# Performance work log

Measured on AMD Instinct MI355X. Metric: run time of the kernel, lower is better.

Reference implementation:

```python
import jax, jax.numpy as jnp
import numpy as np

NEG_MIN = float(np.finfo(np.float32).min)
LN_EPS = 1e-05


def _layer_norm(x, g, b):
    m = jnp.mean(x, axis=-1, keepdims=True)
    v = jnp.var(x, axis=-1, keepdims=True)
    return (x - m) * jax.lax.rsqrt(v + LN_EPS) * g + b


def _rel_shift_uni(x):
    # x: [qlen, rlen, bsz, n_head] -- Transformer-XL relative shift
    q, r, b, n = x.shape
    zero_pad = jnp.zeros((q, 1, b, n), x.dtype)
    x_padded = jnp.concatenate([zero_pad, x], axis=1).reshape(r + 1, q, b, n)
    return x_padded[1:].reshape(q, r, b, n)


def setup_inputs() -> dict:
    key = jax.random.key(0)
    ks = jax.random.split(key, 12)
    qlen, bsz, d_model = 2048, 2, 1024
    n_head, d_head, d_inner = 16, 64, 4096

    w = jax.random.normal(ks[0], (qlen, bsz, d_model), dtype=jnp.float32)

    # sinusoidal relative position embedding, positions klen-1 .. 0
    pos_seq = jnp.arange(qlen - 1, -1, -1, dtype=jnp.float32)
    inv_freq = 1.0 / (10000.0 ** (jnp.arange(0, d_model, 2, dtype=jnp.float32) / d_model))
    sinusoid = pos_seq[:, None] * inv_freq[None, :]
    r = jnp.concatenate([jnp.sin(sinusoid), jnp.cos(sinusoid)], axis=-1)  # [qlen, d_model]

    s = 0.02
    r_w_bias = jax.random.normal(ks[1], (n_head, d_head), dtype=jnp.float32) * s
    r_r_bias = jax.random.normal(ks[2], (n_head, d_head), dtype=jnp.float32) * s
    qkv_w = jax.random.normal(ks[3], (d_model, 3 * n_head * d_head), dtype=jnp.float32) * s
    r_net_w = jax.random.normal(ks[4], (d_model, n_head * d_head), dtype=jnp.float32) * s
    o_w = jax.random.normal(ks[5], (n_head * d_head, d_model), dtype=jnp.float32) * s
    ffn_w1 = jax.random.normal(ks[6], (d_model, d_inner), dtype=jnp.float32) * s
    ffn_b1 = jnp.zeros((d_inner,), dtype=jnp.float32)
    ffn_w2 = jax.random.normal(ks[7], (d_inner, d_model), dtype=jnp.float32) * s
    ffn_b2 = jnp.zeros((d_model,), dtype=jnp.float32)
    ln1_g = jnp.ones((d_model,), dtype=jnp.float32)
    ln1_b = jnp.zeros((d_model,), dtype=jnp.float32)
    ln2_g = jnp.ones((d_model,), dtype=jnp.float32)
    ln2_b = jnp.zeros((d_model,), dtype=jnp.float32)

    # causal mask: position j > i is masked (uni-directional attention)
    attn_mask = jnp.triu(jnp.ones((qlen, qlen), dtype=bool), k=1)

    return {"w": w, "r": r, "r_w_bias": r_w_bias, "r_r_bias": r_r_bias,
            "attn_mask": attn_mask, "qkv_w": qkv_w, "r_net_w": r_net_w, "o_w": o_w,
            "ln1_g": ln1_g, "ln1_b": ln1_b, "ffn_w1": ffn_w1, "ffn_b1": ffn_b1,
            "ffn_w2": ffn_w2, "ffn_b2": ffn_b2, "ln2_g": ln2_g, "ln2_b": ln2_b}


def reference(w, r, r_w_bias, r_r_bias, attn_mask, qkv_w, r_net_w, o_w,
              ln1_g, ln1_b, ffn_w1, ffn_b1, ffn_w2, ffn_b2, ln2_g, ln2_b):
    qlen, bsz, d_model = w.shape
    n_head, d_head = r_w_bias.shape
    scale = 1.0 / (d_head ** 0.5)

    # qkv projection (post-lnorm path: no pre-norm)
    w_heads = w @ qkv_w  # [q, b, 3*n*d]
    w_q, w_k, w_v = jnp.split(w_heads, 3, axis=-1)
    w_q = w_q.reshape(qlen, bsz, n_head, d_head)
    w_k = w_k.reshape(qlen, bsz, n_head, d_head)
    w_v = w_v.reshape(qlen, bsz, n_head, d_head)

    r_k = (r @ r_net_w).reshape(r.shape[0], n_head, d_head)  # [rlen, n, d]

    # AC: content term, BD: position term with rel-shift
    AC = jnp.einsum('ibnd,jbnd->ijbn', w_q + r_w_bias, w_k)
    BD = jnp.einsum('ibnd,jnd->ijbn', w_q + r_r_bias, r_k)
    BD = _rel_shift_uni(BD)

    attn_score = (AC + BD) * scale
    attn_score = jnp.where(attn_mask[:, :, None, None], NEG_MIN, attn_score)
    attn_prob = jax.nn.softmax(attn_score, axis=1)  # softmax over key axis j

    attn_vec = jnp.einsum('ijbn,jbnd->ibnd', attn_prob, w_v)
    attn_vec = attn_vec.reshape(qlen, bsz, n_head * d_head)
    attn_out = attn_vec @ o_w

    x = _layer_norm(w + attn_out, ln1_g, ln1_b)  # post-lnorm

    # PositionwiseFF (post-lnorm, eval: dropout inactive)
    core = jax.nn.relu(x @ ffn_w1 + ffn_b1) @ ffn_w2 + ffn_b2
    out = _layer_norm(x + core, ln2_g, ln2_b)
    return out
```

## Files before the change

kernel.cpp:

```cpp
#include <hip/hip_runtime.h>
#include <math.h>


typedef __attribute__((ext_vector_type(8))) short short8;
typedef __attribute__((ext_vector_type(4))) float floatx4;

__device__ inline unsigned short f2bf(float f) {
  union { float f; unsigned u; } v; v.f = f;
  unsigned r = v.u + 0x7FFFu + ((v.u >> 16) & 1u);
  return (unsigned short)(r >> 16);
}
__device__ inline float bf2f(unsigned short u) {
  union { unsigned u; float f; } v; v.u = ((unsigned)u) << 16; return v.f;
}

#define G2L(gp, lp)                                                  \
  __builtin_amdgcn_global_load_lds(                                  \
      (const __attribute__((address_space(1))) void*)(gp),           \
      (__attribute__((address_space(3))) void*)(lp), 16, 0, 0)

__global__ __launch_bounds__(256) void prep_kernel(
    const float* __restrict__ w, unsigned short* __restrict__ wb,
    const float* __restrict__ r, unsigned short* __restrict__ rb,
    const float* __restrict__ qkv_w, unsigned short* __restrict__ qkvT,
    const float* __restrict__ r_net_w, unsigned short* __restrict__ rnetT,
    const float* __restrict__ o_w, unsigned short* __restrict__ owT,
    const float* __restrict__ ffn_w1, unsigned short* __restrict__ w1T,
    const float* __restrict__ ffn_w2, unsigned short* __restrict__ w2T) {
  __shared__ __align__(16) unsigned short Ts[64][68];
  const int blk = blockIdx.x;
  const int t = threadIdx.x;
  if (blk < 6144) {
    const float* in = blk < 4096 ? w : r;
    unsigned short* outp = blk < 4096 ? wb : rb;
    const int i = (blk < 4096 ? blk : blk - 4096) * 256 + t;
    float4 v = ((const float4*)in)[i];
    ((ushort4*)outp)[i] =
        make_ushort4(f2bf(v.x), f2bf(v.y), f2bf(v.z), f2bf(v.w));
    return;
  }
  const float* src; unsigned short* dst; int K, N, idx;
  if (blk < 6912)      { src = qkv_w;   dst = qkvT;  K = 1024; N = 3072; idx = blk - 6144; }
  else if (blk < 7168) { src = r_net_w; dst = rnetT; K = 1024; N = 1024; idx = blk - 6912; }
  else if (blk < 7424) { src = o_w;     dst = owT;   K = 1024; N = 1024; idx = blk - 7168; }
  else if (blk < 8448) { src = ffn_w1;  dst = w1T;   K = 1024; N = 4096; idx = blk - 7424; }
  else                 { src = ffn_w2;  dst = w2T;   K = 4096; N = 1024; idx = blk - 8448; }
  const int nbx = N >> 6;
  const int k0 = (idx / nbx) * 64, n0 = (idx % nbx) * 64;
  const int rr = t >> 4, c = (t & 15) * 4;
#pragma unroll
  for (int rb2 = 0; rb2 < 64; rb2 += 16) {
    float4 v = *(const float4*)(src + (size_t)(k0 + rb2 + rr) * N + n0 + c);
    *(ushort4*)&Ts[rb2 + rr][c] =
        make_ushort4(f2bf(v.x), f2bf(v.y), f2bf(v.z), f2bf(v.w));
  }
  __syncthreads();
#pragma unroll
  for (int rb2 = 0; rb2 < 64; rb2 += 16) {
    const int nn = rb2 + rr;
    ushort4 o = make_ushort4(Ts[c + 0][nn], Ts[c + 1][nn],
                             Ts[c + 2][nn], Ts[c + 3][nn]);
    *(ushort4*)(dst + (size_t)(n0 + nn) * K + k0 + c) = o;
  }
}

template<int BIAS, int RELU, int OUT_BF16>
__device__ __forceinline__ void bgemm_body(
    const unsigned short* __restrict__ A, const unsigned short* __restrict__ Bt,
    const float* __restrict__ bias, void* __restrict__ C,
    int M, int N, int Kstride, int Klen, size_t psize,
    int bx, int by, int kz,
    unsigned short* As, unsigned short* Bs) {
  const int t = threadIdx.x;
  const int wv = t >> 6, lane = t & 63, quad = lane >> 4, lq = lane & 15;
  const int m0 = by * 128, n0 = bx * 128;
  const int wvm = (wv >> 1) * 64, wvn = (wv & 1) * 64;

  const int srow = t >> 2;
  const int scol = (t & 3) * 8;
  const size_t koff = (size_t)kz * Klen;
  const unsigned short* Ag = A + (size_t)(m0 + srow) * Kstride + scol + koff;
  const unsigned short* Bg = Bt + (size_t)(n0 + srow) * Kstride + scol + koff;
  unsigned short* AsW0 = As + (size_t)wv * 512;
  unsigned short* AsW1 = As + 4096 + (size_t)wv * 512;
  unsigned short* BsW0 = Bs + (size_t)wv * 512;
  unsigned short* BsW1 = Bs + 4096 + (size_t)wv * 512;

  floatx4 acc[4][4];
#pragma unroll
  for (int am = 0; am < 4; ++am)
#pragma unroll
    for (int bn = 0; bn < 4; ++bn) acc[am][bn] = (floatx4){0.f, 0.f, 0.f, 0.f};

  for (int k0 = 0; k0 < Klen; k0 += 64) {
    __syncthreads();
    G2L(Ag + k0, AsW0);
    G2L(Ag + (size_t)64 * Kstride + k0, AsW0 + 64 * 32);
    G2L(Ag + k0 + 32, AsW1);
    G2L(Ag + (size_t)64 * Kstride + k0 + 32, AsW1 + 64 * 32);
    G2L(Bg + k0, BsW0);
    G2L(Bg + (size_t)64 * Kstride + k0, BsW0 + 64 * 32);
    G2L(Bg + k0 + 32, BsW1);
    G2L(Bg + (size_t)64 * Kstride + k0 + 32, BsW1 + 64 * 32);
    __syncthreads();

#pragma unroll
    for (int s = 0; s < 2; ++s) {
      const unsigned short* Asub = s ? As + 4096 : As;
      const unsigned short* Bsub = s ? Bs + 4096 : Bs;
      short8 af[4], bf[4];
#pragma unroll
      for (int am = 0; am < 4; ++am)
        af[am] = *(const short8*)&Asub[(wvm + am * 16 + lq) * 32 + quad * 8];
#pragma unroll
      for (int bn = 0; bn < 4; ++bn)
        bf[bn] = *(const short8*)&Bsub[(wvn + bn * 16 + lq) * 32 + quad * 8];
#pragma unroll
      for (int am = 0; am < 4; ++am)
#pragma unroll
        for (int bn = 0; bn < 4; ++bn)
          acc[am][bn] = __builtin_amdgcn_mfma_f32_16x16x32_bf16(
              af[am], bf[bn], acc[am][bn], 0, 0, 0);
    }
  }

  float bs[4] = {0.f, 0.f, 0.f, 0.f};
  if (BIAS) {
    if (kz == 0) {
#pragma unroll
      for (int bn = 0; bn < 4; ++bn) bs[bn] = bias[n0 + wvn + bn * 16 + lq];
    }
  }
  float* Cf = (float*)C + (size_t)kz * psize;
#pragma unroll
  for (int am = 0; am < 4; ++am) {
#pragma unroll
    for (int u = 0; u < 4; ++u) {
      const size_t row = m0 + wvm + am * 16 + quad * 4 + u;
#pragma unroll
      for (int bn = 0; bn < 4; ++bn) {
        const size_t col = n0 + wvn + bn * 16 + lq;
        float v = acc[am][bn][u];
        if (BIAS) v += bs[bn];
        if (RELU) v = fmaxf(v, 0.f);
        if (OUT_BF16) ((unsigned short*)C)[row * N + col] = f2bf(v);
        else          Cf[row * N + col] = v;
      }
    }
  }
}

template<int BIAS, int RELU, int OUT_BF16>
__global__ __launch_bounds__(256) void bgemm_kernel(
    const unsigned short* __restrict__ A, const unsigned short* __restrict__ Bt,
    const float* __restrict__ bias, void* __restrict__ C,
    int M, int N, int Kstride, int Klen, size_t psize) {
  __shared__ __align__(16) unsigned short As[2 * 128 * 32];
  __shared__ __align__(16) unsigned short Bs[2 * 128 * 32];
  bgemm_body<BIAS, RELU, OUT_BF16>(A, Bt, bias, C, M, N, Kstride, Klen, psize,
                                   blockIdx.x, blockIdx.y, blockIdx.z, As, Bs);
}

template<int BIAS, int RELU, int OUT_BF16>
__device__ __forceinline__ void gemm256_body(
    const unsigned short* __restrict__ A, const unsigned short* __restrict__ Bt,
    const float* __restrict__ bias, void* __restrict__ C,
    int N, int K, int bx, int by,
    unsigned short* As0, unsigned short* As1,
    unsigned short* Bs0, unsigned short* Bs1) {
  const int t = threadIdx.x;
  const int wv = t >> 6, lane = t & 63, quad = lane >> 4, lq = lane & 15;
  const int wr = wv >> 2, wc = wv & 3;
  const int m0 = by * 256, n0 = bx * 256;

  const int srow = t >> 3, scol8 = (t & 7) * 8;
  const unsigned short* Ag = A + (size_t)(m0 + srow) * K + scol8;
  const unsigned short* Bg = Bt + (size_t)(n0 + srow) * K + scol8;

  floatx4 acc[8][4];
#pragma unroll
  for (int am = 0; am < 8; ++am)
#pragma unroll
    for (int bn = 0; bn < 4; ++bn) acc[am][bn] = (floatx4){0.f, 0.f, 0.f, 0.f};

#define STAGE256(Asb, Bsb, k0)                                         \
  do {                                                                 \
    _Pragma("unroll")                                                  \
    for (int i = 0; i < 4; ++i) {                                      \
      G2L(Ag + (size_t)(i * 64) * K + (k0), (Asb) + i * 4096 + wv * 512); \
      G2L(Bg + (size_t)(i * 64) * K + (k0), (Bsb) + i * 4096 + wv * 512); \
    }                                                                  \
  } while (0)

#define COMPUTE256(Asb, Bsb)                                           \
  do {                                                                 \
    _Pragma("unroll")                                                  \
    for (int s = 0; s < 2; ++s) {                                      \
      short8 af[8], bf[4];                                             \
      _Pragma("unroll")                                                \
      for (int am = 0; am < 8; ++am)                                   \
        af[am] = *(const short8*)&(Asb)[(wr * 128 + am * 16 + lq) * 64 + \
                                        s * 32 + quad * 8];            \
      _Pragma("unroll")                                                \
      for (int bn = 0; bn < 4; ++bn)                                   \
        bf[bn] = *(const short8*)&(Bsb)[(wc * 64 + bn * 16 + lq) * 64 + \
                                        s * 32 + quad * 8];            \
      _Pragma("unroll")                                                \
      for (int am = 0; am < 8; ++am)                                   \
        _Pragma("unroll")                                              \
        for (int bn = 0; bn < 4; ++bn)                                 \
          acc[am][bn] = __builtin_amdgcn_mfma_f32_16x16x32_bf16(       \
              af[am], bf[bn], acc[am][bn], 0, 0, 0);                   \
    }                                                                  \
  } while (0)

  const int NT = K >> 6;
  STAGE256(As0, Bs0, 0);
  asm volatile("s_waitcnt vmcnt(0)" ::: "memory");
  __builtin_amdgcn_s_barrier();

  for (int kt = 0; kt + 1 < NT; ++kt) {
    unsigned short* SA = (kt & 1) ? As0 : As1;
    unsigned short* SB = (kt & 1) ? Bs0 : Bs1;
    const unsigned short* CA = (kt & 1) ? As1 : As0;
    const unsigned short* CB = (kt & 1) ? Bs1 : Bs0;
    STAGE256(SA, SB, (kt + 1) * 64);
    COMPUTE256(CA, CB);
    asm volatile("s_waitcnt vmcnt(0)" ::: "memory");
    __builtin_amdgcn_s_barrier();
  }
  if (NT & 1) COMPUTE256(As0, Bs0);
  else        COMPUTE256(As1, Bs1);

#undef STAGE256
#undef COMPUTE256

  float bs[4] = {0.f, 0.f, 0.f, 0.f};
  if (BIAS) {
#pragma unroll
    for (int bn = 0; bn < 4; ++bn) bs[bn] = bias[n0 + wc * 64 + bn * 16 + lq];
  }
#pragma unroll
  for (int am = 0; am < 8; ++am) {
#pragma unroll
    for (int u = 0; u < 4; ++u) {
      const size_t row = m0 + wr * 128 + am * 16 + quad * 4 + u;
#pragma unroll
      for (int bn = 0; bn < 4; ++bn) {
        const size_t col = n0 + wc * 64 + bn * 16 + lq;
        float v = acc[am][bn][u];
        if (BIAS) v += bs[bn];
        if (RELU) v = fmaxf(v, 0.f);
        if (OUT_BF16) ((unsigned short*)C)[row * N + col] = f2bf(v);
        else          ((float*)C)[row * N + col] = v;
      }
    }
  }
}

template<int BIAS, int RELU, int OUT_BF16>
__global__ __launch_bounds__(512, 2) void gemm256_kernel(
    const unsigned short* __restrict__ A, const unsigned short* __restrict__ Bt,
    const float* __restrict__ bias, void* __restrict__ C, int N, int K) {
  __shared__ __align__(16) unsigned short As[2][256 * 64];
  __shared__ __align__(16) unsigned short Bs[2][256 * 64];
  gemm256_body<BIAS, RELU, OUT_BF16>(A, Bt, bias, C, N, K,
                                     blockIdx.x, blockIdx.y,
                                     As[0], As[1], Bs[0], Bs[1]);
}

__global__ __launch_bounds__(512, 2) void qkv_rk256_kernel(
    const unsigned short* __restrict__ wb, const unsigned short* __restrict__ qkvT,
    unsigned short* __restrict__ w_heads,
    const unsigned short* __restrict__ rbf, const unsigned short* __restrict__ rnetT,
    unsigned short* __restrict__ rk) {
  __shared__ __align__(16) unsigned short As[2][256 * 64];
  __shared__ __align__(16) unsigned short Bs[2][256 * 64];
  const int bid = blockIdx.x;
  if (bid < 192) {
    gemm256_body<0, 0, 1>(wb, qkvT, nullptr, w_heads, 3072, 1024,
                          bid % 12, bid / 12, As[0], As[1], Bs[0], Bs[1]);
  } else {
    const int b2 = bid - 192;
    gemm256_body<0, 0, 1>(rbf, rnetT, nullptr, rk, 1024, 1024,
                          b2 % 4, b2 / 4, As[0], As[1], Bs[0], Bs[1]);
  }
}

__global__ __launch_bounds__(512, 4) void attn_mfma_kernel(
    const unsigned short* __restrict__ w_heads,
    const unsigned short* __restrict__ r_k,
    const float* __restrict__ r_w_bias, const float* __restrict__ r_r_bias,
    unsigned short* __restrict__ attn_vec) {
  __shared__ __align__(16) unsigned short Ks[64 * 72];
  __shared__ __align__(16) unsigned short Vt[64 * 72];
  __shared__ __align__(16) unsigned short Rb[256 * 72];
  __shared__ __align__(16) unsigned short Pl[8 * 16 * 72];

  const int t = threadIdx.x;
  const int wv = t >> 6, lane = t & 63, quad = lane >> 4, lq = lane & 15;
  const int g = blockIdx.x;
  const int qq = g >> 5, bnb = g & 31;
  const int it = (qq < 8) ? (15 - qq) : (qq - 8);
  const int b = bnb & 1, n = bnb >> 1;
  const int i0 = it * 128, iw = i0 + wv * 16;

  const int kr = t >> 3, kc8 = (t & 7) * 8;
  const int vj = t & 31, vc = (t >> 5) * 4;

  short8 qw[2], qr[2];
  {
    const unsigned short* qrow =
        w_heads + (size_t)((iw + lq) * 2 + b) * 3072 + n * 64;
    short8 a0 = *(const short8*)(qrow + quad * 8);
    short8 a1 = *(const short8*)(qrow + 32 + quad * 8);
    const float* wbp = r_w_bias + n * 64;
    const float* rbp = r_r_bias + n * 64;
#pragma unroll
    for (int j = 0; j < 8; ++j) {
      const int k0 = quad * 8 + j, k1 = 32 + quad * 8 + j;
      const float q0 = bf2f((unsigned short)a0[j]);
      const float q1 = bf2f((unsigned short)a1[j]);
      qw[0][j] = (short)f2bf(q0 + wbp[k0]);
      qr[0][j] = (short)f2bf(q0 + rbp[k0]);
      qw[1][j] = (short)f2bf(q1 + wbp[k1]);
      qr[1][j] = (short)f2bf(q1 + rbp[k1]);
    }
  }

  floatx4 o[4];
#pragma unroll
  for (int dt = 0; dt < 4; ++dt) o[dt] = (floatx4){0.f, 0.f, 0.f, 0.f};
  float lrow[4] = {0.f, 0.f, 0.f, 0.f};

  unsigned short* Pw = Pl + wv * (16 * 72);
  const int wb2 = 112 - wv * 16;

  int g_idx[4]; bool g_hi[4];
#pragma unroll
  for (int u = 0; u < 4; ++u) {
    const int s = 15 - (quad * 4 + u);
    g_idx[u] = quad * 16 + ((s + lq) & 15);
    g_hi[u] = (s + lq) >= 16;
  }

  const int pbase0 = 1920 - i0;
  const int jt_end = 2 * it + 2;

#pragma unroll
  for (int bq = 0; bq < 2; ++bq) {
    const int row = pbase0 + bq * 64 + kr;
    const int slot = row & 255;
    *(short8*)&Rb[slot * 72 + kc8] =
        *(const short8*)(r_k + (size_t)row * 1024 + n * 64 + kc8);
  }
  short8 sK, sR;
  ushort4 sVl, sVh;
  {
    const unsigned short* kb =
        w_heads + (size_t)(kr * 2 + b) * 3072 + n * 64 + 1024 + kc8;
    sK = *(const short8*)kb;
    const unsigned short* vbp =
        w_heads + (size_t)((2 * vj) * 2 + b) * 3072 + n * 64 + 2048 + vc;
    sVl = *(const ushort4*)vbp;
    sVh = *(const ushort4*)(vbp + 2 * 3072);
    int pg = pbase0 + 128 + kr; if (pg > 2047) pg = 2047;
    sR = *(const short8*)(r_k + (size_t)pg * 1024 + n * 64 + kc8);
  }

  for (int jt = 0; jt < jt_end; ++jt) {
    const int j0 = jt * 64;
    const int pbase = pbase0 + 64 * jt;

    asm volatile("" ::: "memory");
    __builtin_amdgcn_s_barrier();
    asm volatile("" ::: "memory");

    *(short8*)&Ks[kr * 72 + kc8] = sK;
#pragma unroll
    for (int i2 = 0; i2 < 4; ++i2)
      *(unsigned*)&Vt[(vc + i2) * 72 + 2 * vj] =
          (unsigned)sVl[i2] | ((unsigned)sVh[i2] << 16);
    {
      const int slot = (pbase + 128 + kr) & 255;
      *(short8*)&Rb[slot * 72 + kc8] = sR;
    }

    if (jt + 1 < jt_end) {
      const int j0n = j0 + 64;
      const unsigned short* kb =
          w_heads + (size_t)((j0n + kr) * 2 + b) * 3072 + n * 64 + 1024 + kc8;
      sK = *(const short8*)kb;
      const unsigned short* vbp =
          w_heads + (size_t)((j0n + 2 * vj) * 2 + b) * 3072 + n * 64 + 2048 + vc;
      sVl = *(const ushort4*)vbp;
      sVh = *(const ushort4*)(vbp + 2 * 3072);
      int pg = pbase + 192 + kr; if (pg > 2047) pg = 2047;
      sR = *(const short8*)(r_k + (size_t)pg * 1024 + n * 64 + kc8);
    }

    asm volatile("s_waitcnt lgkmcnt(0)" ::: "memory");
    __builtin_amdgcn_s_barrier();
    asm volatile("" ::: "memory");

    floatx4 ac[4];
#pragma unroll
    for (int ct = 0; ct < 4; ++ct) {
      short8 b0 = *(const short8*)&Ks[(ct * 16 + lq) * 72 + quad * 8];
      short8 b1 = *(const short8*)&Ks[(ct * 16 + lq) * 72 + 32 + quad * 8];
      floatx4 z = (floatx4){0.f, 0.f, 0.f, 0.f};
      z = __builtin_amdgcn_mfma_f32_16x16x32_bf16(qw[0], b0, z, 0, 0, 0);
      z = __builtin_amdgcn_mfma_f32_16x16x32_bf16(qw[1], b1, z, 0, 0, 0);
      ac[ct] = z;
    }
    floatx4 Tt[5];
#pragma unroll
    for (int pt = 0; pt < 5; ++pt) {
      const int slot = (pbase + wb2 + pt * 16 + lq) & 255;
      short8 b0 = *(const short8*)&Rb[slot * 72 + quad * 8];
      short8 b1 = *(const short8*)&Rb[slot * 72 + 32 + quad * 8];
      floatx4 z = (floatx4){0.f, 0.f, 0.f, 0.f};
      z = __builtin_amdgcn_mfma_f32_16x16x32_bf16(qr[0], b0, z, 0, 0, 0);
      z = __builtin_amdgcn_mfma_f32_16x16x32_bf16(qr[1], b1, z, 0, 0, 0);
      Tt[pt] = z;
    }

    const bool interior = (j0 + 63 <= iw);
    if (interior) {
#pragma unroll
      for (int u = 0; u < 4; ++u) {
        const int r = quad * 4 + u;
        float sh[5];
#pragma unroll
        for (int pt = 0; pt < 5; ++pt) sh[pt] = __shfl(Tt[pt][u], g_idx[u]);
#pragma unroll
        for (int ct = 0; ct < 4; ++ct) {
          const float bd = g_hi[u] ? sh[ct + 1] : sh[ct];
          const float xs = (ac[ct][u] + bd) * 0.18033688011112042f;
          float pr; asm("v_exp_f32 %0, %1" : "=v"(pr) : "v"(xs));
          Pw[r * 72 + ct * 16 + lq] = f2bf(pr);
          lrow[u] += pr;
        }
      }
    } else {
#pragma unroll
      for (int u = 0; u < 4; ++u) {
        const int r = quad * 4 + u, i = iw + r;
        float sh[5];
#pragma unroll
        for (int pt = 0; pt < 5; ++pt) sh[pt] = __shfl(Tt[pt][u], g_idx[u]);
#pragma unroll
        for (int ct = 0; ct < 4; ++ct) {
          const float bd = g_hi[u] ? sh[ct + 1] : sh[ct];
          const int j = j0 + ct * 16 + lq;
          const float xs = (ac[ct][u] + bd) * 0.18033688011112042f;
          float pr; asm("v_exp_f32 %0, %1" : "=v"(pr) : "v"(xs));
          pr = (j <= i) ? pr : 0.f;
          Pw[r * 72 + ct * 16 + lq] = f2bf(pr);
          lrow[u] += pr;
        }
      }
    }

    __builtin_amdgcn_s_waitcnt(0xC07F);

    short8 pA0 = *(const short8*)&Pw[lq * 72 + quad * 8];
    short8 pA1 = *(const short8*)&Pw[lq * 72 + 32 + quad * 8];
#pragma unroll
    for (int dt = 0; dt < 4; ++dt) {
      short8 v0 = *(const short8*)&Vt[(dt * 16 + lq) * 72 + quad * 8];
      short8 v1 = *(const short8*)&Vt[(dt * 16 + lq) * 72 + 32 + quad * 8];
      o[dt] = __builtin_amdgcn_mfma_f32_16x16x32_bf16(pA0, v0, o[dt], 0, 0, 0);
      o[dt] = __builtin_amdgcn_mfma_f32_16x16x32_bf16(pA1, v1, o[dt], 0, 0, 0);
    }
  }

#pragma unroll
  for (int u = 0; u < 4; ++u) {
    float l = lrow[u];
    l += __shfl_xor(l, 1);
    l += __shfl_xor(l, 2);
    l += __shfl_xor(l, 4);
    l += __shfl_xor(l, 8);
    const float linv = 1.f / l;
    const int i = iw + quad * 4 + u;
    unsigned short* op = attn_vec + (size_t)(i * 2 + b) * 1024 + n * 64 + lq;
#pragma unroll
    for (int dt = 0; dt < 4; ++dt) op[dt * 16] = f2bf(o[dt][u] * linv);
  }
}

__global__ __launch_bounds__(256) void ln_res_kernel(
    const float* __restrict__ X, const float* __restrict__ R0,
    const float* __restrict__ R1,
    const float* __restrict__ g, const float* __restrict__ bta,
    float* __restrict__ out, unsigned short* __restrict__ out_bf) {
  const int row = blockIdx.x;
  const int t = threadIdx.x;
  float4 xv = ((const float4*)(X + (size_t)row * 1024))[t];
  float4 rv = ((const float4*)(R0 + (size_t)row * 1024))[t];
  float4 v = make_float4(xv.x + rv.x, xv.y + rv.y, xv.z + rv.z, xv.w + rv.w);
  if (R1) {
    float4 r2 = ((const float4*)(R1 + (size_t)row * 1024))[t];
    v.x += r2.x; v.y += r2.y; v.z += r2.z; v.w += r2.w;
  }
  float s  = v.x + v.y + v.z + v.w;
  float sq = v.x * v.x + v.y * v.y + v.z * v.z + v.w * v.w;
#pragma unroll
  for (int off = 32; off > 0; off >>= 1) {
    s  += __shfl_xor(s, off);
    sq += __shfl_xor(sq, off);
  }
  __shared__ float ss[4], ssq[4];
  const int wid = t >> 6;
  if ((t & 63) == 0) { ss[wid] = s; ssq[wid] = sq; }
  __syncthreads();
  s  = ss[0] + ss[1] + ss[2] + ss[3];
  sq = ssq[0] + ssq[1] + ssq[2] + ssq[3];
  const float mean = s * (1.f / 1024.f);
  const float var  = sq * (1.f / 1024.f) - mean * mean;
  const float inv  = rsqrtf(var + 1e-5f);
  float4 gv = ((const float4*)g)[t];
  float4 bv = ((const float4*)bta)[t];
  float4 ov = make_float4((v.x - mean) * inv * gv.x + bv.x,
                          (v.y - mean) * inv * gv.y + bv.y,
                          (v.z - mean) * inv * gv.z + bv.z,
                          (v.w - mean) * inv * gv.w + bv.w);
  ((float4*)(out + (size_t)row * 1024))[t] = ov;
  if (out_bf)
    ((ushort4*)(out_bf + (size_t)row * 1024))[t] =
        make_ushort4(f2bf(ov.x), f2bf(ov.y), f2bf(ov.z), f2bf(ov.w));
}

extern "C" void kernel_launch(void* const* d_in, const int* in_sizes, int n_in,
                              void* d_out, int out_size, void* d_ws, size_t ws_size,
                              hipStream_t stream) {
  (void)in_sizes; (void)n_in; (void)out_size; (void)ws_size;
  const float* w        = (const float*)d_in[0];
  const float* r        = (const float*)d_in[1];
  const float* r_w_bias = (const float*)d_in[2];
  const float* r_r_bias = (const float*)d_in[3];
  const float* qkv_w    = (const float*)d_in[5];
  const float* r_net_w  = (const float*)d_in[6];
  const float* o_w      = (const float*)d_in[7];
  const float* ln1_g    = (const float*)d_in[8];
  const float* ln1_b    = (const float*)d_in[9];
  const float* ffn_w1   = (const float*)d_in[10];
  const float* ffn_b1   = (const float*)d_in[11];
  const float* ffn_w2   = (const float*)d_in[12];
  const float* ffn_b2   = (const float*)d_in[13];
  const float* ln2_g    = (const float*)d_in[14];
  const float* ln2_b    = (const float*)d_in[15];
  float* out = (float*)d_out;

  char* base = (char*)d_ws;
  const size_t MB = (size_t)1 << 20;
  unsigned short* w_heads = (unsigned short*)(base + 0);
  float*          aout0   = (float*)(base + 0);
  float*          aout1   = (float*)(base + 16 * MB);
  unsigned short* h1      = (unsigned short*)(base + 0);
  float*          x       = (float*)(base + 32 * MB);
  unsigned short* w2T     = (unsigned short*)(base + 48 * MB);
  unsigned short* w1T     = (unsigned short*)(base + 56 * MB);
  float*          core0   = (float*)(base + 56 * MB);
  float*          core1   = (float*)(base + 72 * MB);
  unsigned short* wb      = (unsigned short*)(base + 64 * MB);
  unsigned short* avec    = (unsigned short*)(base + 64 * MB);
  unsigned short* rb      = (unsigned short*)(base + 72 * MB);
  unsigned short* xb      = (unsigned short*)(base + 72 * MB);
  unsigned short* rk      = (unsigned short*)(base + 76 * MB);
  unsigned short* qkvT    = (unsigned short*)(base + 80 * MB);
  unsigned short* owT     = (unsigned short*)(base + 86 * MB);
  unsigned short* rnetT   = (unsigned short*)(base + 88 * MB);

  dim3 blk(256);
  prep_kernel<<<9472, blk, 0, stream>>>(w, wb, r, rb, qkv_w, qkvT,
                                        r_net_w, rnetT, o_w, owT,
                                        ffn_w1, w1T, ffn_w2, w2T);

  qkv_rk256_kernel<<<224, 512, 0, stream>>>(wb, qkvT, w_heads, rb, rnetT, rk);
  attn_mfma_kernel<<<512, 512, 0, stream>>>(
      w_heads, rk, r_w_bias, r_r_bias, avec);
  bgemm_kernel<0, 0, 0><<<dim3(8, 32, 2), blk, 0, stream>>>(
      avec, owT, nullptr, aout0, 4096, 1024, 1024, 512, (size_t)4096 * 1024);
  ln_res_kernel<<<4096, blk, 0, stream>>>(w, aout0, aout1, ln1_g, ln1_b, x, xb);
  gemm256_kernel<1, 1, 1><<<dim3(16, 16), 512, 0, stream>>>(
      xb, w1T, ffn_b1, h1, 4096, 1024);
  bgemm_kernel<1, 0, 0><<<dim3(8, 32, 2), blk, 0, stream>>>(
      h1, w2T, ffn_b2, core0, 4096, 1024, 4096, 2048, (size_t)4096 * 1024);
  ln_res_kernel<<<4096, blk, 0, stream>>>(x, core0, core1, ln2_g, ln2_b, out, nullptr);
}
```

Measured before the change: 421.6 us.

## Rewrite 256x256 GEMM main loop as fine-grained 8-phase pipeline with LDS swizzle

```diff
diff --git a/kernel.cpp b/kernel.cpp
--- a/kernel.cpp
+++ b/kernel.cpp
@@ -162,20 +162,22 @@
 }
 
 template<int BIAS, int RELU, int OUT_BF16>
-__device__ __forceinline__ void gemm256_body(
+__device__ __forceinline__ void gemm256p8_body(
     const unsigned short* __restrict__ A, const unsigned short* __restrict__ Bt,
     const float* __restrict__ bias, void* __restrict__ C,
     int N, int K, int bx, int by,
-    unsigned short* As0, unsigned short* As1,
-    unsigned short* Bs0, unsigned short* Bs1) {
+    unsigned short* As0, unsigned short* Bs0,
+    unsigned short* As1, unsigned short* Bs1) {
   const int t = threadIdx.x;
   const int wv = t >> 6, lane = t & 63, quad = lane >> 4, lq = lane & 15;
   const int wr = wv >> 2, wc = wv & 3;
   const int m0 = by * 256, n0 = bx * 256;
 
-  const int srow = t >> 3, scol8 = (t & 7) * 8;
-  const unsigned short* Ag = A + (size_t)(m0 + srow) * K + scol8;
-  const unsigned short* Bg = Bt + (size_t)(n0 + srow) * K + scol8;
+  const int srow = t >> 3;
+  const int scol = ((t & 7) * 8) ^ ((t & 32) >> 1);
+  const unsigned short* Ag = A + (size_t)(m0 + srow) * K + scol;
+  const unsigned short* Bg = Bt + (size_t)(n0 + srow) * K + scol;
+  const int c0 = (quad * 8) ^ ((lq & 4) << 2);
 
   floatx4 acc[8][4];
 #pragma unroll
@@ -183,57 +185,99 @@
 #pragma unroll
     for (int bn = 0; bn < 4; ++bn) acc[am][bn] = (floatx4){0.f, 0.f, 0.f, 0.f};
 
-#define STAGE256(Asb, Bsb, k0)                                         \
-  do {                                                                 \
-    _Pragma("unroll")                                                  \
-    for (int i = 0; i < 4; ++i) {                                      \
-      G2L(Ag + (size_t)(i * 64) * K + (k0), (Asb) + i * 4096 + wv * 512); \
-      G2L(Bg + (size_t)(i * 64) * K + (k0), (Bsb) + i * 4096 + wv * 512); \
-    }                                                                  \
+  short8 af[8], bfA[4], bfB[4];
+
+#define STG(dst, gp, rbase, kofs)                                            \
+  do {                                                                       \
+    G2L((gp) + (size_t)(rbase) * K + (kofs), (dst) + (rbase) * 64 + wv * 512); \
+    G2L((gp) + (size_t)((rbase) + 64) * K + (kofs),                          \
+        (dst) + ((rbase) + 64) * 64 + wv * 512);                             \
   } while (0)
 
-#define COMPUTE256(Asb, Bsb)                                           \
-  do {                                                                 \
-    _Pragma("unroll")                                                  \
-    for (int s = 0; s < 2; ++s) {                                      \
-      short8 af[8], bf[4];                                             \
-      _Pragma("unroll")                                                \
-      for (int am = 0; am < 8; ++am)                                   \
-        af[am] = *(const short8*)&(Asb)[(wr * 128 + am * 16 + lq) * 64 + \
-                                        s * 32 + quad * 8];            \
-      _Pragma("unroll")                                                \
-      for (int bn = 0; bn < 4; ++bn)                                   \
-        bf[bn] = *(const short8*)&(Bsb)[(wc * 64 + bn * 16 + lq) * 64 + \
-                                        s * 32 + quad * 8];            \
-      _Pragma("unroll")                                                \
-      for (int am = 0; am < 8; ++am)                                   \
-        _Pragma("unroll")                                              \
-        for (int bn = 0; bn < 4; ++bn)                                 \
-          acc[am][bn] = __builtin_amdgcn_mfma_f32_16x16x32_bf16(       \
-              af[am], bf[bn], acc[am][bn], 0, 0, 0);                   \
-    }                                                                  \
-  } while (0)
-
-  const int NT = K >> 6;
-  STAGE256(As0, Bs0, 0);
-  asm volatile("s_waitcnt vmcnt(0)" ::: "memory");
-  __builtin_amdgcn_s_barrier();
-
-  for (int kt = 0; kt + 1 < NT; ++kt) {
-    unsigned short* SA = (kt & 1) ? As0 : As1;
-    unsigned short* SB = (kt & 1) ? Bs0 : Bs1;
-    const unsigned short* CA = (kt & 1) ? As1 : As0;
-    const unsigned short* CB = (kt & 1) ? Bs1 : Bs0;
-    STAGE256(SA, SB, (kt + 1) * 64);
-    COMPUTE256(CA, CB);
-    asm volatile("s_waitcnt vmcnt(0)" ::: "memory");
-    __builtin_amdgcn_s_barrier();
-  }
-  if (NT & 1) COMPUTE256(As0, Bs0);
-  else        COMPUTE256(As1, Bs1);
-
-#undef STAGE256
-#undef COMPUTE256
+#define LDAF(buf, ah)                                                        \
+  _Pragma("unroll")                                                          \
+  for (int i_ = 0; i_ < 4; ++i_) {                                           \
+    const int ar_ = (wr * 128 + (ah) * 64 + i_ * 16 + lq) * 64;              \
+    af[i_ * 2 + 0] = *(const short8*)&(buf)[ar_ + c0];                       \
+    af[i_ * 2 + 1] = *(const short8*)&(buf)[ar_ + 32 + c0];                  \
+  }
+
+#define LDBF(dst, buf, bh)                                                   \
+  _Pragma("unroll")                                                          \
+  for (int i_ = 0; i_ < 2; ++i_) {                                           \
+    const int br_ = (wc * 64 + (bh) * 32 + i_ * 16 + lq) * 64;               \
+    dst[i_ * 2 + 0] = *(const short8*)&(buf)[br_ + c0];                      \
+    dst[i_ * 2 + 1] = *(const short8*)&(buf)[br_ + 32 + c0];                 \
+  }
+
+#define MM(ah, bh, bfX)                                                      \
+  __builtin_amdgcn_s_setprio(1);                                             \
+  _Pragma("unroll")                                                          \
+  for (int i_ = 0; i_ < 4; ++i_)                                             \
+    _Pragma("unroll")                                                        \
+    for (int j_ = 0; j_ < 2; ++j_) {                                         \
+      acc[(ah) * 4 + i_][(bh) * 2 + j_] =                                    \
+          __builtin_amdgcn_mfma_f32_16x16x32_bf16(                           \
+              af[i_ * 2 + 0], bfX[j_ * 2 + 0],                               \
+              acc[(ah) * 4 + i_][(bh) * 2 + j_], 0, 0, 0);                   \
+      acc[(ah) * 4 + i_][(bh) * 2 + j_] =                                    \
+          __builtin_amdgcn_mfma_f32_16x16x32_bf16(                           \
+              af[i_ * 2 + 1], bfX[j_ * 2 + 1],                               \
+              acc[(ah) * 4 + i_][(bh) * 2 + j_], 0, 0, 0);                   \
+    }                                                                        \
+  __builtin_amdgcn_s_setprio(0);
+
+#define BAR() __builtin_amdgcn_s_barrier()
+#define VM2() asm volatile("s_waitcnt vmcnt(2)" ::: "memory")
+#define VM0() asm volatile("s_waitcnt vmcnt(0)" ::: "memory")
+
+  const int NI = K >> 7;
+
+  STG(As0, Ag, 0, 0);   STG(Bs0, Bg, 0, 0);
+  STG(As0, Ag, 128, 0); STG(Bs0, Bg, 128, 0);
+  STG(As1, Ag, 0, 64);
+  VM2();
+  BAR();
+
+  for (int it = 0; it < NI; ++it) {
+    const int ke = it * 128;
+    const bool stg = (it + 1 < NI);
+
+    LDAF(As0, 0); LDBF(bfA, Bs0, 0);
+    STG(Bs1, Bg, 0, ke + 64);
+    BAR(); MM(0, 0, bfA); BAR();
+    LDBF(bfB, Bs0, 1);
+    STG(As1, Ag, 128, ke + 64);
+    BAR(); MM(0, 1, bfB); BAR();
+    LDAF(As0, 1);
+    STG(Bs1, Bg, 128, ke + 64);
+    BAR(); MM(1, 1, bfB); BAR();
+    if (stg) STG(As0, Ag, 0, ke + 128);
+    BAR(); MM(1, 0, bfA);
+    if (stg) VM2(); else VM0();
+    BAR();
+    LDAF(As1, 0); LDBF(bfA, Bs1, 0);
+    if (stg) STG(Bs0, Bg, 0, ke + 128);
+    BAR(); MM(0, 0, bfA); BAR();
+    LDBF(bfB, Bs1, 1);
+    if (stg) STG(As0, Ag, 128, ke + 128);
+    BAR(); MM(0, 1, bfB); BAR();
+    LDAF(As1, 1);
+    if (stg) STG(Bs0, Bg, 128, ke + 128);
+    BAR(); MM(1, 1, bfB); BAR();
+    if (stg) STG(As1, Ag, 0, ke + 192);
+    BAR(); MM(1, 0, bfA);
+    if (stg) VM2(); else VM0();
+    BAR();
+  }
+
+#undef STG
+#undef LDAF
+#undef LDBF
+#undef MM
+#undef BAR
+#undef VM2
+#undef VM0
 
   float bs[4] = {0.f, 0.f, 0.f, 0.f};
   if (BIAS) {
@@ -259,14 +303,14 @@
 }
 
 template<int BIAS, int RELU, int OUT_BF16>
-__global__ __launch_bounds__(512, 2) void gemm256_kernel(
+__global__ __launch_bounds__(512, 2) void gemm256p8_kernel(
     const unsigned short* __restrict__ A, const unsigned short* __restrict__ Bt,
     const float* __restrict__ bias, void* __restrict__ C, int N, int K) {
   __shared__ __align__(16) unsigned short As[2][256 * 64];
   __shared__ __align__(16) unsigned short Bs[2][256 * 64];
-  gemm256_body<BIAS, RELU, OUT_BF16>(A, Bt, bias, C, N, K,
-                                     blockIdx.x, blockIdx.y,
-                                     As[0], As[1], Bs[0], Bs[1]);
+  gemm256p8_body<BIAS, RELU, OUT_BF16>(A, Bt, bias, C, N, K,
+                                       blockIdx.x, blockIdx.y,
+                                       As[0], Bs[0], As[1], Bs[1]);
 }
 
 __global__ __launch_bounds__(512, 2) void qkv_rk256_kernel(
@@ -278,12 +322,12 @@
   __shared__ __align__(16) unsigned short Bs[2][256 * 64];
   const int bid = blockIdx.x;
   if (bid < 192) {
-    gemm256_body<0, 0, 1>(wb, qkvT, nullptr, w_heads, 3072, 1024,
-                          bid % 12, bid / 12, As[0], As[1], Bs[0], Bs[1]);
+    gemm256p8_body<0, 0, 1>(wb, qkvT, nullptr, w_heads, 3072, 1024,
+                            bid % 12, bid / 12, As[0], Bs[0], As[1], Bs[1]);
   } else {
     const int b2 = bid - 192;
-    gemm256_body<0, 0, 1>(rbf, rnetT, nullptr, rk, 1024, 1024,
-                          b2 % 4, b2 / 4, As[0], As[1], Bs[0], Bs[1]);
+    gemm256p8_body<0, 0, 1>(rbf, rnetT, nullptr, rk, 1024, 1024,
+                            b2 % 4, b2 / 4, As[0], Bs[0], As[1], Bs[1]);
   }
 }
 
@@ -584,7 +628,7 @@
   bgemm_kernel<0, 0, 0><<<dim3(8, 32, 2), blk, 0, stream>>>(
       avec, owT, nullptr, aout0, 4096, 1024, 1024, 512, (size_t)4096 * 1024);
   ln_res_kernel<<<4096, blk, 0, stream>>>(w, aout0, aout1, ln1_g, ln1_b, x, xb);
-  gemm256_kernel<1, 1, 1><<<dim3(16, 16), 512, 0, stream>>>(
+  gemm256p8_kernel<1, 1, 1><<<dim3(16, 16), 512, 0, stream>>>(
       xb, w1T, ffn_b1, h1, 4096, 1024);
   bgemm_kernel<1, 0, 0><<<dim3(8, 32, 2), blk, 0, stream>>>(
       h1, w2T, ffn_b2, core0, 4096, 1024, 4096, 2048, (size_t)4096 * 1024);
```

Result: faster. 413.1 us (-2.0%).
